# Performance work log

Hardware: AMD Instinct MI355X
Metric: run time of the kernel (lower is better)

The kernel has to match this reference:

```python
import jax, jax.numpy as jnp
import numpy as np

B, L, M, H = 16, 1024, 1024, 128
NEG = -1e30


def setup_inputs() -> dict:
    key = jax.random.key(0)
    ks = jax.random.split(key, 8)
    return {
        "text": jax.random.normal(ks[0], (B, L, H), dtype=jnp.float32),
        "modality": jax.random.normal(ks[1], (B, M, H), dtype=jnp.float32),
        "text_mask": jax.random.randint(ks[2], (B, L), 0, 2, dtype=jnp.int32),
        "modality_mask": jax.random.randint(ks[3], (B, M), 0, 2, dtype=jnp.int32),
        # learned parameters (xavier-uniform style scale)
        "text_weight": jax.random.normal(ks[4], (H, 1), dtype=jnp.float32) * 0.1,
        "modality_weight": jax.random.normal(ks[5], (H, 1), dtype=jnp.float32) * 0.1,
        "text_modality_weight": jax.random.normal(ks[6], (1, 1, H), dtype=jnp.float32) * 0.1,
        "bias": jnp.zeros((1,), dtype=jnp.float32),
    }


def reference(text, modality, text_mask, modality_mask,
              text_weight, modality_weight, text_modality_weight, bias):
    # similarity matrix s: (B, L, M)   (eval mode: dropout is identity)
    s0 = jnp.matmul(text, text_weight)                      # (B, L, 1)
    s1 = jnp.swapaxes(jnp.matmul(modality, modality_weight), 1, 2)  # (B, 1, M)
    s2 = jnp.einsum('blh,bmh->blm', text * text_modality_weight, modality)
    s = s0 + s1 + s2 + bias                                 # (B, L, M)

    mmask = modality_mask[:, None, :].astype(jnp.float32)   # (B, 1, M)
    tmask = text_mask[:, :, None].astype(jnp.float32)       # (B, L, 1)
    p1 = jax.nn.softmax(mmask * s + (1.0 - mmask) * NEG, axis=2)  # text->modality
    p2 = jax.nn.softmax(tmask * s + (1.0 - tmask) * NEG, axis=1)  # modality->text

    a = jnp.matmul(p1, modality)                            # (B, L, H)
    b = jnp.matmul(jnp.matmul(p1, jnp.swapaxes(p2, 1, 2)), text)  # (B, L, H)
    return jnp.concatenate([text, a, text * a, text * b], axis=2)  # (B, L, 8H)
```

## Files before the change

### kernel.cpp

```cpp
#include <hip/hip_runtime.h>

#define B_ 16
#define L_ 1024
#define M_ 1024
#define H_ 128

typedef unsigned short u16;
typedef unsigned int u32;
typedef __bf16 bf16x8 __attribute__((ext_vector_type(8)));
typedef float f32x4 __attribute__((ext_vector_type(4)));

__device__ __forceinline__ u16 f2bf(float x){
  u32 u = __float_as_uint(x);
  u = (u + 0x7fffu + ((u >> 16) & 1u)) >> 16;
  return (u16)u;
}

__device__ __forceinline__ void gload16(const u16* g, char* l) {
  __builtin_amdgcn_global_load_lds(
      (const __attribute__((address_space(1))) u32*)(const void*)g,
      (__attribute__((address_space(3))) u32*)(void*)l, 16, 0, 0);
}

__global__ __launch_bounds__(256) void prep2(
    const float* __restrict__ text, const float* __restrict__ modality,
    const int* __restrict__ tmask, const int* __restrict__ mmask,
    const float* __restrict__ tw, const float* __restrict__ mw,
    const float* __restrict__ tmw,
    u16* __restrict__ textw_bf, u16* __restrict__ mod_bf,
    u16* __restrict__ textT_bf, u16* __restrict__ modT_bf,
    float* __restrict__ t0, float* __restrict__ s1m,
    float4* __restrict__ zbase, int n4)
{
  for (int i = blockIdx.x * 256 + threadIdx.x; i < n4; i += 512 * 256)
    zbase[i] = make_float4(0.f, 0.f, 0.f, 0.f);

  int g = blockIdx.x;
  int sel = g >> 8;
  int b = (g >> 4) & 15;
  int r0 = (g & 15) * 64;
  const float* src = (sel ? modality : text) + ((size_t)b * 1024 + r0) * H_;
  const int* msk = (sel ? mmask : tmask) + b * 1024 + r0;
  const float* dotw = sel ? mw : tw;
  u16* rowout = (sel ? mod_bf : textw_bf) + ((size_t)b * 1024 + r0) * H_;
  u16* trout = (sel ? modT_bf : textT_bf) + (size_t)b * H_ * 1024 + r0;
  float* dotout = (sel ? s1m : t0) + b * 1024 + r0;

  __shared__ u16 tile[128][72];
  int tid = threadIdx.x;
  int rgrp = tid >> 5;
  int lane32 = tid & 31;
  int h0 = lane32 * 4;
  float4 w4 = *(const float4*)&dotw[h0];
  float4 mv = sel ? make_float4(1.f, 1.f, 1.f, 1.f) : *(const float4*)&tmw[h0];
  float dpart[8];
  #pragma unroll
  for (int p = 0; p < 8; p++) {
    int row = rgrp + p * 8;
    float4 x = *(const float4*)&src[(size_t)row * H_ + h0];
    dpart[p] = x.x * w4.x + x.y * w4.y + x.z * w4.z + x.w * w4.w;
    uint2 pk;
    pk.x = (u32)f2bf(x.x * mv.x) | ((u32)f2bf(x.y * mv.y) << 16);
    pk.y = (u32)f2bf(x.z * mv.z) | ((u32)f2bf(x.w * mv.w) << 16);
    *(uint2*)&rowout[(size_t)row * H_ + h0] = pk;
    int mk = msk[row];
    tile[h0 + 0][row] = mk ? f2bf(x.x) : (u16)0;
    tile[h0 + 1][row] = mk ? f2bf(x.y) : (u16)0;
    tile[h0 + 2][row] = mk ? f2bf(x.z) : (u16)0;
    tile[h0 + 3][row] = mk ? f2bf(x.w) : (u16)0;
  }
  #pragma unroll
  for (int p = 0; p < 8; p++) {
    float d = dpart[p];
    #pragma unroll
    for (int off = 1; off < 32; off <<= 1) d += __shfl_xor(d, off);
    if (lane32 == 0) dotout[rgrp + p * 8] = d;
  }
  __syncthreads();
  int lcol = (tid & 7) * 8;
  #pragma unroll
  for (int p = 0; p < 4; p++) {
    int h = (tid >> 3) + p * 32;
    uint4 v = *(const uint4*)&tile[h][lcol];
    *(uint4*)&trout[(size_t)h * 1024 + lcol] = v;
  }
}

__global__ __launch_bounds__(256) void gemm_exp(
    const u16* __restrict__ A, const u16* __restrict__ Bm,
    const float* __restrict__ t0, const float* __restrict__ s1m,
    const float* __restrict__ bias, const int* __restrict__ tmask,
    const int* __restrict__ mmask, float* __restrict__ rowsum,
    float* __restrict__ colsum, u16* __restrict__ ET)
{
  int f = blockIdx.x;
  int orig = (f & 7) * 256 + (f >> 3);
  int b = orig >> 7;
  int a0 = (orig & 15) * 64, b0 = ((orig >> 4) & 7) * 128;
  int tid = threadIdx.x, lane = tid & 63, wid = tid >> 6;
  int wr = wid >> 1, wc = wid & 1;
  int c = lane & 15, q = lane >> 4;
  __shared__ __align__(16) char smem[24576];
  const u16* Ab = A + (size_t)(b * L_ + a0) * H_;
  const u16* Bb = Bm + (size_t)(b * M_ + b0) * H_;
  int rsub = lane >> 3;
  int scol8 = (lane & 7) ^ rsub;
  f32x4 acc[2][4];
  #pragma unroll
  for (int i = 0; i < 2; i++)
    #pragma unroll
    for (int j = 0; j < 4; j++) acc[i][j] = (f32x4){0.f, 0.f, 0.f, 0.f};
  for (int kt = 0; kt < 2; kt++) {
    __syncthreads();
    #pragma unroll
    for (int i = 0; i < 2; i++)
      gload16(Ab + (size_t)(wid * 8 + i * 32 + rsub) * H_ + kt * 64 + scol8 * 8,
              smem + wid * 1024 + i * 4096);
    #pragma unroll
    for (int i = 0; i < 4; i++)
      gload16(Bb + (size_t)(wid * 8 + i * 32 + rsub) * H_ + kt * 64 + scol8 * 8,
              smem + 8192 + wid * 1024 + i * 4096);
    __syncthreads();
    #pragma unroll
    for (int kk = 0; kk < 2; kk++) {
      int kbyte = kk * 64 + (q << 4);
      bf16x8 af[2], bfr[4];
      #pragma unroll
      for (int i = 0; i < 2; i++) {
        int ra = wr * 32 + i * 16 + c;
        af[i] = *(const bf16x8*)(smem + ra * 128 + (kbyte ^ ((ra & 7) << 4)));
      }
      #pragma unroll
      for (int j = 0; j < 4; j++) {
        int rb = wc * 64 + j * 16 + c;
        bfr[j] = *(const bf16x8*)(smem + 8192 + rb * 128 + (kbyte ^ ((rb & 7) << 4)));
      }
      #pragma unroll
      for (int i = 0; i < 2; i++)
        #pragma unroll
        for (int j = 0; j < 4; j++)
          acc[i][j] = __builtin_amdgcn_mfma_f32_16x16x32_bf16(af[i], bfr[j], acc[i][j], 0, 0, 0);
    }
  }
  float biasv = bias[0];
  float t0v[2][4];
  int tmv[2][4];
  #pragma unroll
  for (int i = 0; i < 2; i++)
    #pragma unroll
    for (int r = 0; r < 4; r++) {
      int ar = a0 + wr * 32 + i * 16 + q * 4 + r;
      t0v[i][r] = t0[b * L_ + ar];
      tmv[i][r] = tmask[b * L_ + ar];
    }
  float s1v[4];
  int mmv[4];
  #pragma unroll
  for (int j = 0; j < 4; j++) {
    int gcol = b0 + wc * 64 + j * 16 + c;
    s1v[j] = s1m[b * M_ + gcol];
    mmv[j] = mmask[b * M_ + gcol];
  }
  float ev[2][4][4];
  #pragma unroll
  for (int i = 0; i < 2; i++)
    #pragma unroll
    for (int j = 0; j < 4; j++)
      #pragma unroll
      for (int r = 0; r < 4; r++)
        ev[i][j][r] = __expf(acc[i][j][r] + t0v[i][r] + s1v[j] + biasv);
  #pragma unroll
  for (int i = 0; i < 2; i++)
    #pragma unroll
    for (int r = 0; r < 4; r++) {
      float prs = 0.f;
      #pragma unroll
      for (int j = 0; j < 4; j++) prs += mmv[j] ? ev[i][j][r] : 0.f;
      #pragma unroll
      for (int off = 1; off < 16; off <<= 1) prs += __shfl_xor(prs, off);
      if (c == 0) {
        int ar = a0 + wr * 32 + i * 16 + q * 4 + r;
        atomicAdd(&rowsum[b * L_ + ar], prs);
      }
    }
  #pragma unroll
  for (int j = 0; j < 4; j++) {
    float pcs = 0.f;
    #pragma unroll
    for (int i = 0; i < 2; i++)
      #pragma unroll
      for (int r = 0; r < 4; r++) pcs += tmv[i][r] ? ev[i][j][r] : 0.f;
    pcs += __shfl_xor(pcs, 16);
    pcs += __shfl_xor(pcs, 32);
    if (q == 0) {
      int gcol = b0 + wc * 64 + j * 16 + c;
      atomicAdd(&colsum[b * M_ + gcol], pcs);
    }
  }
  __syncthreads();
  u16* et = (u16*)smem;
  #pragma unroll
  for (int i = 0; i < 2; i++)
    #pragma unroll
    for (int j = 0; j < 4; j++) {
      int gcolL = wc * 64 + j * 16 + c;
      int arL = wr * 32 + i * 16 + q * 4;
      u32 lo = (u32)f2bf(ev[i][j][0]) | ((u32)f2bf(ev[i][j][1]) << 16);
      u32 hi = (u32)f2bf(ev[i][j][2]) | ((u32)f2bf(ev[i][j][3]) << 16);
      uint2 pk; pk.x = lo; pk.y = hi;
      *(uint2*)&et[gcolL * 72 + arL] = pk;
    }
  __syncthreads();
  #pragma unroll
  for (int it = 0; it < 4; it++) {
    int mrow = (tid >> 3) + it * 32;
    int l8 = tid & 7;
    uint4 v = *(const uint4*)&et[mrow * 72 + l8 * 8];
    *(uint4*)&ET[((size_t)(b * M_ + b0 + mrow)) * L_ + a0 + l8 * 8] = v;
  }
}

__global__ __launch_bounds__(512) void gemm_ct(
    const u16* __restrict__ A, const u16* __restrict__ ET,
    float* __restrict__ c_f32)
{
  int f = blockIdx.x;
  int orig = (f & 7) * 64 + (f >> 3);
  int b = orig >> 5;
  int x = orig & 3, y = (orig >> 2) & 7;
  int ia = x & 1, ks = x >> 1;
  int a0 = ia * 64, b0 = y * 128;
  int tid = threadIdx.x, lane = tid & 63, wid = tid >> 6;
  int wr = wid >> 2, wc = wid & 3;
  int c = lane & 15, q = lane >> 4;
  __shared__ __align__(16) char smem[24576];
  const u16* Ab = A + (size_t)(b * H_ + a0) * L_;
  const u16* Bb = ET + (size_t)(b * M_ + b0) * L_;
  int sRow = tid >> 3, sCol8 = tid & 7;
  int swzA = sRow * 128 + ((sCol8 * 16) ^ ((sRow & 7) << 4));
  f32x4 acc[2][2];
  #pragma unroll
  for (int i = 0; i < 2; i++)
    #pragma unroll
    for (int j = 0; j < 2; j++) acc[i][j] = (f32x4){0.f, 0.f, 0.f, 0.f};

  uint4 rA, rB0, rB1;
  auto LOAD = [&](int kt) {
    rA = *(const uint4*)(Ab + (size_t)sRow * L_ + kt * 64 + sCol8 * 8);
    rB0 = *(const uint4*)(Bb + (size_t)sRow * L_ + kt * 64 + sCol8 * 8);
    rB1 = *(const uint4*)(Bb + (size_t)(sRow + 64) * L_ + kt * 64 + sCol8 * 8);
  };
  auto WRITE = [&]() {
    *(uint4*)(smem + swzA) = rA;
    *(uint4*)(smem + 8192 + swzA) = rB0;
    *(uint4*)(smem + 8192 + 8192 + swzA) = rB1;
  };
  int kt0 = ks * 8;
  LOAD(kt0);
  WRITE();
  for (int t = 0; t < 8; t++) {
    if (t < 7) LOAD(kt0 + t + 1);
    __syncthreads();
    #pragma unroll
    for (int kk = 0; kk < 2; kk++) {
      int kbyte = kk * 64 + (q << 4);
      bf16x8 af[2], bfr[2];
      #pragma unroll
      for (int i = 0; i < 2; i++) {
        int ra = wr * 32 + i * 16 + c;
        af[i] = *(const bf16x8*)(smem + ra * 128 + (kbyte ^ ((ra & 7) << 4)));
      }
      #pragma unroll
      for (int j = 0; j < 2; j++) {
        int rb = wc * 32 + j * 16 + c;
        bfr[j] = *(const bf16x8*)(smem + 8192 + rb * 128 + (kbyte ^ ((rb & 7) << 4)));
      }
      #pragma unroll
      for (int i = 0; i < 2; i++)
        #pragma unroll
        for (int j = 0; j < 2; j++)
          acc[i][j] = __builtin_amdgcn_mfma_f32_16x16x32_bf16(af[i], bfr[j], acc[i][j], 0, 0, 0);
    }
    __syncthreads();
    if (t < 7) WRITE();
  }
  #pragma unroll
  for (int i = 0; i < 2; i++)
    #pragma unroll
    for (int j = 0; j < 2; j++) {
      int arow0 = a0 + wr * 32 + i * 16 + q * 4;
      int gcol = b0 + wc * 32 + j * 16 + c;
      #pragma unroll
      for (int r = 0; r < 4; r++)
        atomicAdd(&c_f32[((size_t)(b * H_ + arow0 + r)) * M_ + gcol], acc[i][j][r]);
    }
}

__global__ __launch_bounds__(1024) void gemm_ab(
    const u16* __restrict__ ET, const u16* __restrict__ B1,
    const float* __restrict__ c_f32, const float* __restrict__ colsum,
    const int* __restrict__ mmask, const float* __restrict__ rowsum,
    const float* __restrict__ text, float* __restrict__ out)
{
  int f = blockIdx.x;
  int orig = (f & 7) * 32 + (f >> 3);
  int b = orig >> 4;
  int a0 = (orig & 15) * 64;
  int tid = threadIdx.x, lane = tid & 63, wid = tid >> 6;
  int wr = wid >> 3, wc = wid & 7;
  int c = lane & 15, q = lane >> 4;
  __shared__ __align__(16) u16 At[64 * 76];
  __shared__ __align__(16) char Bs[2][16384];
  __shared__ float invcm[1024];
  const u16* ETb = ET + (size_t)b * M_ * L_;
  const u16* B1b = B1 + (size_t)b * H_ * M_;
  const float* cfb = c_f32 + (size_t)b * H_ * M_;
  invcm[tid] = mmask[b * M_ + tid] ? 1.0f / fmaxf(colsum[b * M_ + tid], 1e-30f) : 0.f;

  int sArow = tid >> 4, sAcol = (tid & 15) * 4;
  int sBrow = tid >> 3, sBcol8 = tid & 7;

  f32x4 acc_a[2], acc_b[2];
  #pragma unroll
  for (int i = 0; i < 2; i++) {
    acc_a[i] = (f32x4){0.f, 0.f, 0.f, 0.f};
    acc_b[i] = (f32x4){0.f, 0.f, 0.f, 0.f};
  }

  uint2 rA;
  uint4 rB1;
  float4 rB2a, rB2b;
  auto LOAD = [&](int kt) {
    rA = *(const uint2*)&ETb[((size_t)(kt * 64 + sArow)) * L_ + a0 + sAcol];
    int mbase = kt * 64 + sBcol8 * 8;
    rB1 = *(const uint4*)(B1b + (size_t)sBrow * M_ + mbase);
    rB2a = *(const float4*)&cfb[(size_t)sBrow * M_ + mbase];
    rB2b = *(const float4*)&cfb[(size_t)sBrow * M_ + mbase + 4];
  };
  auto WRITE = [&](int kt) {
    *(uint2*)(At + sArow * 76 + sAcol) = rA;
    int swz = (sBcol8 * 16) ^ ((sBrow & 7) << 4);
    *(uint4*)(Bs[0] + sBrow * 128 + swz) = rB1;
    int mbase = kt * 64 + sBcol8 * 8;
    float4 ia4 = *(const float4*)&invcm[mbase];
    float4 ib4 = *(const float4*)&invcm[mbase + 4];
    uint4 v2;
    v2.x = (u32)f2bf(rB2a.x * ia4.x) | ((u32)f2bf(rB2a.y * ia4.y) << 16);
    v2.y = (u32)f2bf(rB2a.z * ia4.z) | ((u32)f2bf(rB2a.w * ia4.w) << 16);
    v2.z = (u32)f2bf(rB2b.x * ib4.x) | ((u32)f2bf(rB2b.y * ib4.y) << 16);
    v2.w = (u32)f2bf(rB2b.z * ib4.z) | ((u32)f2bf(rB2b.w * ib4.w) << 16);
    *(uint4*)(Bs[1] + sBrow * 128 + swz) = v2;
  };

  LOAD(0);
  __syncthreads();
  WRITE(0);
  for (int kt = 0; kt < 16; kt++) {
    if (kt < 15) LOAD(kt + 1);
    __syncthreads();
    #pragma unroll
    for (int kk = 0; kk < 2; kk++) {
      int kbyte = kk * 64 + (q << 4);
      bf16x8 af[2], b1f, b2f;
      #pragma unroll
      for (int i = 0; i < 2; i++) {
        int lidx = wr * 32 + i * 16 + c;
        int mbase = kk * 32 + q * 8;
        union { unsigned short s[8]; bf16x8 v; } ua;
        #pragma unroll
        for (int e = 0; e < 8; e++) ua.s[e] = At[(mbase + e) * 76 + lidx];
        af[i] = ua.v;
      }
      int rb = wc * 16 + c;
      b1f = *(const bf16x8*)(Bs[0] + rb * 128 + (kbyte ^ ((rb & 7) << 4)));
      b2f = *(const bf16x8*)(Bs[1] + rb * 128 + (kbyte ^ ((rb & 7) << 4)));
      #pragma unroll
      for (int i = 0; i < 2; i++) {
        acc_a[i] = __builtin_amdgcn_mfma_f32_16x16x32_bf16(af[i], b1f, acc_a[i], 0, 0, 0);
        acc_b[i] = __builtin_amdgcn_mfma_f32_16x16x32_bf16(af[i], b2f, acc_b[i], 0, 0, 0);
      }
    }
    __syncthreads();
    if (kt < 15) WRITE(kt + 1);
  }

  float irs[2][4];
  #pragma unroll
  for (int i = 0; i < 2; i++)
    #pragma unroll
    for (int r = 0; r < 4; r++) {
      int ar = a0 + wr * 32 + i * 16 + q * 4 + r;
      irs[i][r] = 1.0f / fmaxf(rowsum[b * L_ + ar], 1e-30f);
    }
  int gcol = wc * 16 + c;
  #pragma unroll
  for (int i = 0; i < 2; i++) {
    #pragma unroll
    for (int r = 0; r < 4; r++) {
      int ar = a0 + wr * 32 + i * 16 + q * 4 + r;
      float av = acc_a[i][r] * irs[i][r];
      float bv = acc_b[i][r] * irs[i][r];
      float tv = text[((size_t)(b * L_ + ar)) * H_ + gcol];
      size_t base = ((size_t)(b * L_ + ar)) * 512 + gcol;
      out[base] = tv;
      out[base + 128] = av;
      out[base + 256] = tv * av;
      out[base + 384] = tv * bv;
    }
  }
}

extern "C" void kernel_launch(void* const* d_in, const int* in_sizes, int n_in,
                              void* d_out, int out_size, void* d_ws, size_t ws_size,
                              hipStream_t stream) {
  const float* text = (const float*)d_in[0];
  const float* modality = (const float*)d_in[1];
  const int* text_mask = (const int*)d_in[2];
  const int* modality_mask = (const int*)d_in[3];
  const float* text_weight = (const float*)d_in[4];
  const float* modality_weight = (const float*)d_in[5];
  const float* tmw = (const float*)d_in[6];
  const float* bias = (const float*)d_in[7];
  float* out = (float*)d_out;
  (void)in_sizes; (void)n_in; (void)out_size; (void)ws_size;

  char* ws = (char*)d_ws;
  size_t off = 0;
  auto alloc = [&](size_t bytes) { void* p = ws + off; off += (bytes + 255) & ~(size_t)255; return p; };
  u16*   ET       = (u16*)  alloc((size_t)B_ * M_ * L_ * 2);
  u16*   textw_bf = (u16*)  alloc((size_t)B_ * L_ * H_ * 2);
  u16*   mod_bf   = (u16*)  alloc((size_t)B_ * M_ * H_ * 2);
  u16*   textT_bf = (u16*)  alloc((size_t)B_ * H_ * L_ * 2);
  u16*   mod_bfT  = (u16*)  alloc((size_t)B_ * H_ * M_ * 2);
  float* t0       = (float*)alloc((size_t)B_ * L_ * 4);
  float* s1m      = (float*)alloc((size_t)B_ * M_ * 4);
  float* rowsum   = (float*)alloc((size_t)B_ * L_ * 4);
  float* colsum   = (float*)alloc((size_t)B_ * M_ * 4);
  float* c_f32    = (float*)alloc((size_t)B_ * H_ * M_ * 4);

  int n4 = (B_ * (L_ + M_) + B_ * H_ * M_) / 4;
  prep2<<<512, 256, 0, stream>>>(text, modality, text_mask, modality_mask,
      text_weight, modality_weight, tmw,
      textw_bf, mod_bf, textT_bf, mod_bfT, t0, s1m, (float4*)rowsum, n4);
  gemm_exp<<<2048, 256, 0, stream>>>(textw_bf, mod_bf, t0, s1m, bias,
      text_mask, modality_mask, rowsum, colsum, ET);
  gemm_ct<<<512, 512, 0, stream>>>(textT_bf, ET, c_f32);
  gemm_ab<<<256, 1024, 0, stream>>>(ET, mod_bfT, c_f32, colsum, modality_mask,
      rowsum, text, out);
}
```

Baseline: 160.2 us.

## Drop split-K atomics in gemm_ct and emit normalized bf16 C directly

gemm_ct now runs the full K=1024 per block instead of a 2-way split-K, so it writes its output directly rather than through float atomicAdd. It applies the column mask and inverse column-sum scaling in its epilogue and stores bf16, so gemm_ab loads bf16 tiles without doing conversion or normalization. This removes the zeroing of the c_f32 buffer in prep2, the atomic traffic, and half the read bytes in gemm_ab. The cost is that gemm_ct launches half as many blocks (256) with a k-loop twice as long, which lowers parallelism on the GPU.

```diff
diff --git a/kernel.cpp b/kernel.cpp
--- a/kernel.cpp
+++ b/kernel.cpp
@@ -222,14 +222,14 @@
 
 __global__ __launch_bounds__(512) void gemm_ct(
     const u16* __restrict__ A, const u16* __restrict__ ET,
-    float* __restrict__ c_f32)
+    const int* __restrict__ mmask, const float* __restrict__ colsum,
+    u16* __restrict__ cT)
 {
   int f = blockIdx.x;
-  int orig = (f & 7) * 64 + (f >> 3);
-  int b = orig >> 5;
-  int x = orig & 3, y = (orig >> 2) & 7;
-  int ia = x & 1, ks = x >> 1;
-  int a0 = ia * 64, b0 = y * 128;
+  int orig = (f & 7) * 32 + (f >> 3);
+  int b = orig >> 4;
+  int rem = orig & 15;
+  int a0 = (rem & 1) * 64, b0 = (rem >> 1) * 128;
   int tid = threadIdx.x, lane = tid & 63, wid = tid >> 6;
   int wr = wid >> 2, wc = wid & 3;
   int c = lane & 15, q = lane >> 4;
@@ -255,11 +255,10 @@
     *(uint4*)(smem + 8192 + swzA) = rB0;
     *(uint4*)(smem + 8192 + 8192 + swzA) = rB1;
   };
-  int kt0 = ks * 8;
-  LOAD(kt0);
+  LOAD(0);
   WRITE();
-  for (int t = 0; t < 8; t++) {
-    if (t < 7) LOAD(kt0 + t + 1);
+  for (int t = 0; t < 16; t++) {
+    if (t < 15) LOAD(t + 1);
     __syncthreads();
     #pragma unroll
     for (int kk = 0; kk < 2; kk++) {
@@ -282,7 +281,13 @@
           acc[i][j] = __builtin_amdgcn_mfma_f32_16x16x32_bf16(af[i], bfr[j], acc[i][j], 0, 0, 0);
     }
     __syncthreads();
-    if (t < 7) WRITE();
+    if (t < 15) WRITE();
+  }
+  float invc[2];
+  #pragma unroll
+  for (int j = 0; j < 2; j++) {
+    int gcol = b0 + wc * 32 + j * 16 + c;
+    invc[j] = mmask[b * M_ + gcol] ? 1.0f / fmaxf(colsum[b * M_ + gcol], 1e-30f) : 0.f;
   }
   #pragma unroll
   for (int i = 0; i < 2; i++)
@@ -292,14 +297,13 @@
       int gcol = b0 + wc * 32 + j * 16 + c;
       #pragma unroll
       for (int r = 0; r < 4; r++)
-        atomicAdd(&c_f32[((size_t)(b * H_ + arow0 + r)) * M_ + gcol], acc[i][j][r]);
+        cT[((size_t)(b * H_ + arow0 + r)) * M_ + gcol] = f2bf(acc[i][j][r] * invc[j]);
     }
 }
 
 __global__ __launch_bounds__(1024) void gemm_ab(
     const u16* __restrict__ ET, const u16* __restrict__ B1,
-    const float* __restrict__ c_f32, const float* __restrict__ colsum,
-    const int* __restrict__ mmask, const float* __restrict__ rowsum,
+    const u16* __restrict__ B2, const float* __restrict__ rowsum,
     const float* __restrict__ text, float* __restrict__ out)
 {
   int f = blockIdx.x;
@@ -311,14 +315,13 @@
   int c = lane & 15, q = lane >> 4;
   __shared__ __align__(16) u16 At[64 * 76];
   __shared__ __align__(16) char Bs[2][16384];
-  __shared__ float invcm[1024];
   const u16* ETb = ET + (size_t)b * M_ * L_;
   const u16* B1b = B1 + (size_t)b * H_ * M_;
-  const float* cfb = c_f32 + (size_t)b * H_ * M_;
-  invcm[tid] = mmask[b * M_ + tid] ? 1.0f / fmaxf(colsum[b * M_ + tid], 1e-30f) : 0.f;
+  const u16* B2b = B2 + (size_t)b * H_ * M_;
 
   int sArow = tid >> 4, sAcol = (tid & 15) * 4;
   int sBrow = tid >> 3, sBcol8 = tid & 7;
+  int swzB = sBrow * 128 + ((sBcol8 * 16) ^ ((sBrow & 7) << 4));
 
   f32x4 acc_a[2], acc_b[2];
   #pragma unroll
@@ -328,33 +331,21 @@
   }
 
   uint2 rA;
-  uint4 rB1;
-  float4 rB2a, rB2b;
+  uint4 rB1, rB2;
   auto LOAD = [&](int kt) {
     rA = *(const uint2*)&ETb[((size_t)(kt * 64 + sArow)) * L_ + a0 + sAcol];
     int mbase = kt * 64 + sBcol8 * 8;
     rB1 = *(const uint4*)(B1b + (size_t)sBrow * M_ + mbase);
-    rB2a = *(const float4*)&cfb[(size_t)sBrow * M_ + mbase];
-    rB2b = *(const float4*)&cfb[(size_t)sBrow * M_ + mbase + 4];
+    rB2 = *(const uint4*)(B2b + (size_t)sBrow * M_ + mbase);
   };
-  auto WRITE = [&](int kt) {
+  auto WRITE = [&]() {
     *(uint2*)(At + sArow * 76 + sAcol) = rA;
-    int swz = (sBcol8 * 16) ^ ((sBrow & 7) << 4);
-    *(uint4*)(Bs[0] + sBrow * 128 + swz) = rB1;
-    int mbase = kt * 64 + sBcol8 * 8;
-    float4 ia4 = *(const float4*)&invcm[mbase];
-    float4 ib4 = *(const float4*)&invcm[mbase + 4];
-    uint4 v2;
-    v2.x = (u32)f2bf(rB2a.x * ia4.x) | ((u32)f2bf(rB2a.y * ia4.y) << 16);
-    v2.y = (u32)f2bf(rB2a.z * ia4.z) | ((u32)f2bf(rB2a.w * ia4.w) << 16);
-    v2.z = (u32)f2bf(rB2b.x * ib4.x) | ((u32)f2bf(rB2b.y * ib4.y) << 16);
-    v2.w = (u32)f2bf(rB2b.z * ib4.z) | ((u32)f2bf(rB2b.w * ib4.w) << 16);
-    *(uint4*)(Bs[1] + sBrow * 128 + swz) = v2;
+    *(uint4*)(Bs[0] + swzB) = rB1;
+    *(uint4*)(Bs[1] + swzB) = rB2;
   };
 
   LOAD(0);
-  __syncthreads();
-  WRITE(0);
+  WRITE();
   for (int kt = 0; kt < 16; kt++) {
     if (kt < 15) LOAD(kt + 1);
     __syncthreads();
@@ -381,7 +372,7 @@
       }
     }
     __syncthreads();
-    if (kt < 15) WRITE(kt + 1);
+    if (kt < 15) WRITE();
   }
 
   float irs[2][4];
@@ -432,19 +423,18 @@
   u16*   mod_bf   = (u16*)  alloc((size_t)B_ * M_ * H_ * 2);
   u16*   textT_bf = (u16*)  alloc((size_t)B_ * H_ * L_ * 2);
   u16*   mod_bfT  = (u16*)  alloc((size_t)B_ * H_ * M_ * 2);
+  u16*   cT       = (u16*)  alloc((size_t)B_ * H_ * M_ * 2);
   float* t0       = (float*)alloc((size_t)B_ * L_ * 4);
   float* s1m      = (float*)alloc((size_t)B_ * M_ * 4);
   float* rowsum   = (float*)alloc((size_t)B_ * L_ * 4);
   float* colsum   = (float*)alloc((size_t)B_ * M_ * 4);
-  float* c_f32    = (float*)alloc((size_t)B_ * H_ * M_ * 4);
-
-  int n4 = (B_ * (L_ + M_) + B_ * H_ * M_) / 4;
+
+  int n4 = (B_ * (L_ + M_)) / 4;
   prep2<<<512, 256, 0, stream>>>(text, modality, text_mask, modality_mask,
       text_weight, modality_weight, tmw,
       textw_bf, mod_bf, textT_bf, mod_bfT, t0, s1m, (float4*)rowsum, n4);
   gemm_exp<<<2048, 256, 0, stream>>>(textw_bf, mod_bf, t0, s1m, bias,
       text_mask, modality_mask, rowsum, colsum, ET);
-  gemm_ct<<<512, 512, 0, stream>>>(textT_bf, ET, c_f32);
-  gemm_ab<<<256, 1024, 0, stream>>>(ET, mod_bfT, c_f32, colsum, modality_mask,
-      rowsum, text, out);
-}
+  gemm_ct<<<256, 512, 0, stream>>>(textT_bf, ET, modality_mask, colsum, cT);
+  gemm_ab<<<256, 1024, 0, stream>>>(ET, mod_bfT, cT, rowsum, text, out);
+}
```

After: 145.6 us. 1.1x faster.
